# Kernel optimization log

Measured on AMD Instinct MI355X. Metric: run time of the kernel, lower is better.

The kernel has to match this reference:

```python
import jax, jax.numpy as jnp
import numpy as np

N = 50000       # nodes
E = 800000      # edges (avg degree 16)
F_IN = 128      # in_feats
H = 128         # h_feats
C = 16          # num_classes
EPS = 1e-5      # BatchNorm eps


def setup_inputs() -> dict:
    key = jax.random.key(0)
    ks = jax.random.split(key, 26)
    rn = lambda k, shape: jax.random.normal(k, shape, dtype=jnp.float32) * 0.05
    zeros = lambda d: jnp.zeros((d,), jnp.float32)
    ones = lambda d: jnp.ones((d,), jnp.float32)
    return {
        "features": jax.random.normal(ks[0], (N, F_IN), dtype=jnp.float32),
        "src": jax.random.randint(ks[1], (E,), 0, N),
        "dst": jax.random.randint(ks[2], (E,), 0, N),
        # input_encoder
        "W_in": rn(ks[3], (F_IN, H)), "b_in": zeros(H),
        # SAGEConv layer 0: H -> 2H (fc_self, fc_neigh, bias)
        "Ws0": rn(ks[4], (H, 2 * H)), "Wn0": rn(ks[5], (H, 2 * H)), "bs0": zeros(2 * H),
        # BatchNorm1d(2H) eval-mode stats
        "g0": ones(2 * H), "bt0": zeros(2 * H),
        "m0": rn(ks[6], (2 * H,)),
        "v0": jax.random.uniform(ks[7], (2 * H,), jnp.float32, 0.5, 1.5),
        # SAGEConv layer 1: 2H -> H
        "Ws1": rn(ks[8], (2 * H, H)), "Wn1": rn(ks[9], (2 * H, H)), "bs1": zeros(H),
        # BatchNorm1d(H)
        "g1": ones(H), "bt1": zeros(H),
        "m1": rn(ks[10], (H,)),
        "v1": jax.random.uniform(ks[11], (H,), jnp.float32, 0.5, 1.5),
        # relation_encoder: 2H -> H
        "Wr": rn(ks[12], (2 * H, H)), "br": zeros(H),
        # classifier: H -> H//2 -> C
        "Wc1": rn(ks[13], (H, H // 2)), "bc1": zeros(H // 2),
        "Wc2": rn(ks[14], (H // 2, C)), "bc2": zeros(C),
    }


def _bn(x, g, b, m, v):
    # eval-mode BatchNorm1d with running stats
    return (x - m) * jax.lax.rsqrt(v + EPS) * g + b


def _sage(h, src, dst, Ws, Wn, b, inv_deg):
    # DGL SAGEConv 'mean': out = fc_self(h_dst) + fc_neigh(mean_{u in N(v)} h_u) + bias
    neigh = jax.ops.segment_sum(h[src], dst, num_segments=N) * inv_deg  # [N, d_in]
    return h @ Ws + neigh @ Wn + b


def reference(features, src, dst, W_in, b_in, Ws0, Wn0, bs0, g0, bt0, m0, v0,
              Ws1, Wn1, bs1, g1, bt1, m1, v1, Wr, br, Wc1, bc1, Wc2, bc2):
    deg = jax.ops.segment_sum(jnp.ones((E,), jnp.float32), dst, num_segments=N)
    inv_deg = (1.0 / jnp.maximum(deg, 1.0))[:, None]  # [N, 1]

    h0 = jax.nn.relu(features @ W_in + b_in)                       # [N, H]
    h = jax.nn.relu(_bn(_sage(h0, src, dst, Ws0, Wn0, bs0, inv_deg), g0, bt0, m0, v0))  # [N, 2H]
    h = jax.nn.relu(_bn(_sage(h, src, dst, Ws1, Wn1, bs1, inv_deg), g1, bt1, m1, v1))   # [N, H]

    h_final = jax.nn.relu(jnp.concatenate([h0, h], axis=1) @ Wr + br)  # [N, H]
    return jax.nn.relu(h_final @ Wc1 + bc1) @ Wc2 + bc2                # [N, C]
```

## Files before the change

### kernel.cpp

```cpp
#include <hip/hip_runtime.h>

typedef short v8s __attribute__((ext_vector_type(8)));
typedef float v4f __attribute__((ext_vector_type(4)));
typedef unsigned short u16;
typedef unsigned int u32;

#define NNODES 50000
#define NEDGES 800000
#define CSTRIDE 64

#define NB 512
#define BSPAN 98
#define EBLK 98
#define NBU 511
#define SUBCAP 48

__device__ __forceinline__ float bf2f(u16 b) {
    u32 u = ((u32)b) << 16;
    return __builtin_bit_cast(float, u);
}
__device__ __forceinline__ u16 f2bf(float f) {
    u32 u = __builtin_bit_cast(u32, f);
    u32 r = (u + 0x7fffu + ((u >> 16) & 1u)) >> 16;
    return (u16)r;
}

struct PackDesc { const float* B1; const float* B2; int K1, K2, N, csplit, start; u16* out; };
struct PackArgs { PackDesc d[6]; int total; };

__global__ __launch_bounds__(256) void prep_pack(
    PackArgs pa,
    const float* b_in, const float* bs0, const float* g0, const float* bt0,
    const float* m0, const float* v0,
    const float* bs1, const float* g1, const float* bt1, const float* m1, const float* v1,
    const float* br, const float* bc1, const float* bc2,
    float* sc_in, float* sh_in, float* sc0, float* sh0, float* sc1, float* sh1,
    float* sc_r, float* sh_r, float* sh_c1, float* sh_c2) {
    int t = threadIdx.x;
    if (blockIdx.x == 0) {
        if (t < 128) { sc_in[t] = 1.f; sh_in[t] = b_in[t]; }
        if (t < 256) {
            float s = g0[t] * rsqrtf(v0[t] + 1e-5f);
            sc0[t] = s;
            sh0[t] = (bs0[t] - m0[t]) * s + bt0[t];
        }
        if (t < 128) {
            float s = g1[t] * rsqrtf(v1[t] + 1e-5f);
            sc1[t] = s;
            sh1[t] = (bs1[t] - m1[t]) * s + bt1[t];
        }
        if (t < 128) { sc_r[t] = 1.f; sh_r[t] = br[t]; }
        if (t < 64)  { sh_c1[t] = bc1[t]; }
        if (t < 16)  { sh_c2[t] = bc2[t]; }
    }
    int tid = blockIdx.x * 256 + t;
    if (tid >= pa.total) return;
    int s = 0;
    for (int i = 1; i < 6; i++)
        if (tid >= pa.d[i].start) s = i;
    const PackDesc& D = pa.d[s];
    int tt = tid - D.start;
    int frag = tt >> 9;
    int rem = tt & 511;
    int lane = rem >> 3;
    int j = rem & 7;
    int nf = D.N >> 4;
    int kt = frag / nf, nt = frag - kt * nf;
    int k = kt * 32 + (lane >> 4) * 8 + j;
    int n = nt * 16 + (lane & 15);
    float v;
    if (D.csplit)
        v = (n < D.csplit) ? D.B1[(size_t)k * D.csplit + n]
                           : D.B2[(size_t)k * (D.N - D.csplit) + (n - D.csplit)];
    else
        v = (k < D.K1) ? D.B1[(size_t)k * D.N + n]
                       : D.B2[(size_t)(k - D.K1) * D.N + n];
    D.out[tt] = f2bf(v);
}

template <int BN, int CW, int KT, int KSPLIT, bool RELU, bool F32OUT, bool AF32>
__device__ __forceinline__ void gemm_body(
    int bx,
    const void* __restrict__ A0v, int lda0,
    const void* __restrict__ A1v, int lda1,
    int M,
    const v8s* __restrict__ Bp,
    const float* __restrict__ scale, const float* __restrict__ shift,
    u16* __restrict__ C, float* __restrict__ Cf, int ldc) {
    constexpr int NFW = BN / 16 / CW;
    constexpr int RW = 4 / CW;
    int lane = threadIdx.x & 63;
    int wave = threadIdx.x >> 6;
    int colw = wave % CW;
    int roww = wave / CW;
    int quad = lane >> 4;
    int l16 = lane & 15;
    int base = bx * (64 * RW) + roww * 64;

    v4f acc[4][NFW];
#pragma unroll
    for (int rg = 0; rg < 4; rg++)
#pragma unroll
        for (int nt = 0; nt < NFW; nt++) acc[rg][nt] = (v4f)0.0f;

    size_t o0[4], o1[4];
#pragma unroll
    for (int rg = 0; rg < 4; rg++) {
        int r = base + rg * 16 + l16;
        if (r > M - 1) r = M - 1;
        o0[rg] = (size_t)r * lda0 + quad * 8;
        o1[rg] = (size_t)r * lda1 + quad * 8;
    }

    auto load_a = [&](const void* Av, size_t off) -> v8s {
        if constexpr (AF32) {
            const float* p = (const float*)Av + off;
            float4 x = *(const float4*)p;
            float4 y = *(const float4*)(p + 4);
            v8s a;
            a[0] = (short)f2bf(x.x); a[1] = (short)f2bf(x.y);
            a[2] = (short)f2bf(x.z); a[3] = (short)f2bf(x.w);
            a[4] = (short)f2bf(y.x); a[5] = (short)f2bf(y.y);
            a[6] = (short)f2bf(y.z); a[7] = (short)f2bf(y.w);
            return a;
        } else {
            return *(const v8s*)((const u16*)Av + off);
        }
    };

#pragma unroll
    for (int kt = 0; kt < KT; kt++) {
        v8s a[4];
#pragma unroll
        for (int rg = 0; rg < 4; rg++) {
            if (kt < KSPLIT) a[rg] = load_a(A0v, o0[rg] + kt * 32);
            else             a[rg] = load_a(A1v, o1[rg] + (size_t)(kt - KSPLIT) * 32);
        }
        const v8s* bb = Bp + (size_t)kt * (BN / 16) * 64 + (colw * NFW) * 64 + lane;
#pragma unroll
        for (int nt = 0; nt < NFW; nt++) {
            v8s b = bb[nt * 64];
#pragma unroll
            for (int rg = 0; rg < 4; rg++)
                acc[rg][nt] = __builtin_amdgcn_mfma_f32_16x16x32_bf16(a[rg], b, acc[rg][nt], 0, 0, 0);
        }
    }

    int colbase = colw * (NFW * 16);
#pragma unroll
    for (int rg = 0; rg < 4; rg++) {
        int rbase = base + rg * 16 + quad * 4;
#pragma unroll
        for (int nt = 0; nt < NFW; nt++) {
            int col = colbase + nt * 16 + l16;
            float s = scale[col], sh = shift[col];
#pragma unroll
            for (int i = 0; i < 4; i++) {
                int row = rbase + i;
                if (row < M) {
                    float v = acc[rg][nt][i] * s + sh;
                    if (RELU) v = v > 0.f ? v : 0.f;
                    if (F32OUT) Cf[(size_t)row * ldc + col] = v;
                    else C[(size_t)row * ldc + col] = f2bf(v);
                }
            }
        }
    }
}

__device__ __forceinline__ u32 gather_mean2(
    const u16* __restrict__ nl, int d, const u16* __restrict__ Hl, int ldh) {
    float a0 = 0.f, a1 = 0.f, b0 = 0.f, b1 = 0.f;
    float c0 = 0.f, c1 = 0.f, d0 = 0.f, d1 = 0.f;
    float e0 = 0.f, e1 = 0.f, f0 = 0.f, f1 = 0.f;
    float g0 = 0.f, g1 = 0.f, h0_ = 0.f, h1_ = 0.f;
    int e = 0;
    for (; e + 8 <= d; e += 8) {
        int u0 = nl[e], u1 = nl[e + 1], u2 = nl[e + 2], u3 = nl[e + 3];
        int u4 = nl[e + 4], u5 = nl[e + 5], u6 = nl[e + 6], u7 = nl[e + 7];
        u32 w0 = *(const u32*)(Hl + (size_t)u0 * ldh);
        u32 w1 = *(const u32*)(Hl + (size_t)u1 * ldh);
        u32 w2 = *(const u32*)(Hl + (size_t)u2 * ldh);
        u32 w3 = *(const u32*)(Hl + (size_t)u3 * ldh);
        u32 w4 = *(const u32*)(Hl + (size_t)u4 * ldh);
        u32 w5 = *(const u32*)(Hl + (size_t)u5 * ldh);
        u32 w6 = *(const u32*)(Hl + (size_t)u6 * ldh);
        u32 w7 = *(const u32*)(Hl + (size_t)u7 * ldh);
        a0 += bf2f((u16)w0); a1 += bf2f((u16)(w0 >> 16));
        b0 += bf2f((u16)w1); b1 += bf2f((u16)(w1 >> 16));
        c0 += bf2f((u16)w2); c1 += bf2f((u16)(w2 >> 16));
        d0 += bf2f((u16)w3); d1 += bf2f((u16)(w3 >> 16));
        e0 += bf2f((u16)w4); e1 += bf2f((u16)(w4 >> 16));
        f0 += bf2f((u16)w5); f1 += bf2f((u16)(w5 >> 16));
        g0 += bf2f((u16)w6); g1 += bf2f((u16)(w6 >> 16));
        h0_ += bf2f((u16)w7); h1_ += bf2f((u16)(w7 >> 16));
    }
    for (; e + 4 <= d; e += 4) {
        int u0 = nl[e], u1 = nl[e + 1], u2 = nl[e + 2], u3 = nl[e + 3];
        u32 w0 = *(const u32*)(Hl + (size_t)u0 * ldh);
        u32 w1 = *(const u32*)(Hl + (size_t)u1 * ldh);
        u32 w2 = *(const u32*)(Hl + (size_t)u2 * ldh);
        u32 w3 = *(const u32*)(Hl + (size_t)u3 * ldh);
        a0 += bf2f((u16)w0); a1 += bf2f((u16)(w0 >> 16));
        b0 += bf2f((u16)w1); b1 += bf2f((u16)(w1 >> 16));
        c0 += bf2f((u16)w2); c1 += bf2f((u16)(w2 >> 16));
        d0 += bf2f((u16)w3); d1 += bf2f((u16)(w3 >> 16));
    }
    for (; e < d; e++) {
        int u = nl[e];
        u32 w = *(const u32*)(Hl + (size_t)u * ldh);
        a0 += bf2f((u16)w); a1 += bf2f((u16)(w >> 16));
    }
    float s = 1.0f / (float)(d > 0 ? d : 1);
    float r0 = ((a0 + b0) + (c0 + d0)) + ((e0 + f0) + (g0 + h0_));
    float r1 = ((a1 + b1) + (c1 + d1)) + ((e1 + f1) + (g1 + h1_));
    return (u32)f2bf(r0 * s) | ((u32)f2bf(r1 * s) << 16);
}

__global__ __launch_bounds__(256) void mega_binA_h0(
    const int* __restrict__ src, const int* __restrict__ dst,
    int* __restrict__ gcnt, u32* __restrict__ gbuf,
    const float* __restrict__ features,
    const v8s* __restrict__ Winp,
    const float* __restrict__ sc_in, const float* __restrict__ sh_in,
    u16* __restrict__ hcat0) {
    int bx = blockIdx.x;
    if (bx < EBLK) {
        __shared__ int lcnt[NB];
        int t = threadIdx.x;
        for (int i = t; i < NB; i += 256) lcnt[i] = 0;
        __syncthreads();
        int ebase = bx * 8192;
#pragma unroll
        for (int c = 0; c < 8; c++) {
            int e0 = ebase + c * 1024 + t * 4;
            if (e0 + 4 <= NEDGES) {
                int4 s4 = *(const int4*)(src + e0);
                int4 d4 = *(const int4*)(dst + e0);
                int ss[4] = {s4.x, s4.y, s4.z, s4.w};
                int dd[4] = {d4.x, d4.y, d4.z, d4.w};
#pragma unroll
                for (int j = 0; j < 4; j++) {
                    int b = dd[j] / BSPAN;
                    int dl = dd[j] - b * BSPAN;
                    int p = atomicAdd(&lcnt[b], 1);
                    if (p < SUBCAP)
                        gbuf[((size_t)b * EBLK + bx) * SUBCAP + p] =
                            ((u32)dl << 16) | (u32)ss[j];
                }
            } else {
#pragma unroll
                for (int j = 0; j < 4; j++) {
                    int e = e0 + j;
                    if (e < NEDGES) {
                        int d = dst[e];
                        int b = d / BSPAN;
                        int dl = d - b * BSPAN;
                        int p = atomicAdd(&lcnt[b], 1);
                        if (p < SUBCAP)
                            gbuf[((size_t)b * EBLK + bx) * SUBCAP + p] =
                                ((u32)dl << 16) | (u32)src[e];
                    }
                }
            }
        }
        __syncthreads();
        for (int i = t; i < NB; i += 256) {
            int c = lcnt[i];
            if (c > SUBCAP) c = SUBCAP;
            gcnt[bx * NB + i] = c;
        }
    } else {
        gemm_body<128, 4, 4, 4, true, false, true>(
            bx - EBLK, features, 128, features, 128, NNODES,
            Winp, sc_in, sh_in, hcat0, nullptr, 256);
    }
}

__global__ __launch_bounds__(1024) void fill_bg(
    const u32* __restrict__ gbuf, const int* __restrict__ gcnt,
    u16* __restrict__ csr, int* __restrict__ cursor,
    const u16* __restrict__ H, u16* __restrict__ D) {
    __shared__ u16 lcsr[BSPAN * CSTRIDE];
    __shared__ int lcur[BSPAN];
    __shared__ int scnt[EBLK];
    int b = blockIdx.x;
    int t = threadIdx.x;
    int v0 = b * BSPAN;
    int span = NNODES - v0;
    if (span > BSPAN) span = BSPAN;
    for (int i = t; i < BSPAN; i += 1024) lcur[i] = 0;
    for (int i = t; i < EBLK; i += 1024) scnt[i] = gcnt[i * NB + b];
    __syncthreads();
    const u32* gb = gbuf + (size_t)b * EBLK * SUBCAP;
    for (int s = t; s < EBLK * SUBCAP; s += 1024) {
        int blk = s / SUBCAP;
        int idx = s - blk * SUBCAP;
        if (idx < scnt[blk]) {
            u32 pk = gb[s];
            int dl = pk >> 16;
            int p = atomicAdd(&lcur[dl], 1);
            if (p < CSTRIDE) lcsr[(dl << 6) + p] = (u16)(pk & 0xffffu);
        }
    }
    __syncthreads();
    {
        const u32* lw = (const u32*)lcsr;
        u32* gw = (u32*)(csr + ((size_t)v0 << 6));
        int nw = span * (CSTRIDE / 2);
        for (int i = t; i < nw; i += 1024) gw[i] = lw[i];
        for (int i = t; i < span; i += 1024) cursor[v0 + i] = lcur[i];
    }
    int lane = t & 63;
    int wv = t >> 6;
    for (int i = wv; i < span; i += 16) {
        int d = lcur[i];
        if (d > CSTRIDE) d = CSTRIDE;
        u32 o = gather_mean2(&lcsr[i << 6], d, H + lane * 2, 256);
        *(u32*)(D + (size_t)(v0 + i) * 256 + lane * 2) = o;
    }
}

__global__ __launch_bounds__(256) void gemm_h1ps(
    const u16* __restrict__ A,
    const v8s* __restrict__ B0,
    const float* __restrict__ sc0, const float* __restrict__ sh0,
    const v8s* __restrict__ B1,
    u16* __restrict__ ps, int M) {
    constexpr int LSTR = 264;
    __shared__ u16 h1s[64 * LSTR];
    int lane = threadIdx.x & 63;
    int wave = threadIdx.x >> 6;
    int quad = lane >> 4;
    int l16 = lane & 15;
    int base = blockIdx.x * 64;

    v4f acc[4][4];
#pragma unroll
    for (int rg = 0; rg < 4; rg++)
#pragma unroll
        for (int nt = 0; nt < 4; nt++) acc[rg][nt] = (v4f)0.0f;

    size_t o0[4];
#pragma unroll
    for (int rg = 0; rg < 4; rg++) {
        int r = base + rg * 16 + l16;
        if (r > M - 1) r = M - 1;
        o0[rg] = (size_t)r * 256 + quad * 8;
    }

#pragma unroll
    for (int kt = 0; kt < 8; kt++) {
        v8s a[4];
#pragma unroll
        for (int rg = 0; rg < 4; rg++) a[rg] = *(const v8s*)(A + o0[rg] + kt * 32);
        const v8s* bb = B0 + (size_t)kt * 16 * 64 + (wave * 4) * 64 + lane;
#pragma unroll
        for (int nt = 0; nt < 4; nt++) {
            v8s b = bb[nt * 64];
#pragma unroll
            for (int rg = 0; rg < 4; rg++)
                acc[rg][nt] = __builtin_amdgcn_mfma_f32_16x16x32_bf16(a[rg], b, acc[rg][nt], 0, 0, 0);
        }
    }
    int colbase = wave * 64;
#pragma unroll
    for (int rg = 0; rg < 4; rg++) {
        int rowL = rg * 16 + quad * 4;
#pragma unroll
        for (int nt = 0; nt < 4; nt++) {
            int col = colbase + nt * 16 + l16;
            float s = sc0[col], sh = sh0[col];
#pragma unroll
            for (int i = 0; i < 4; i++) {
                float v = acc[rg][nt][i] * s + sh;
                v = v > 0.f ? v : 0.f;
                h1s[(rowL + i) * LSTR + col] = f2bf(v);
            }
        }
    }
    __syncthreads();

#pragma unroll
    for (int rg = 0; rg < 4; rg++)
#pragma unroll
        for (int nt = 0; nt < 4; nt++) acc[rg][nt] = (v4f)0.0f;
#pragma unroll
    for (int kt = 0; kt < 8; kt++) {
        v8s a[4];
#pragma unroll
        for (int rg = 0; rg < 4; rg++)
            a[rg] = *(const v8s*)(&h1s[(rg * 16 + l16) * LSTR + quad * 8 + kt * 32]);
        const v8s* bb = B1 + (size_t)kt * 16 * 64 + (wave * 4) * 64 + lane;
#pragma unroll
        for (int nt = 0; nt < 4; nt++) {
            v8s b = bb[nt * 64];
#pragma unroll
            for (int rg = 0; rg < 4; rg++)
                acc[rg][nt] = __builtin_amdgcn_mfma_f32_16x16x32_bf16(a[rg], b, acc[rg][nt], 0, 0, 0);
        }
    }
#pragma unroll
    for (int rg = 0; rg < 4; rg++) {
        int rbase = base + rg * 16 + quad * 4;
#pragma unroll
        for (int nt = 0; nt < 4; nt++) {
            int col = colbase + nt * 16 + l16;
#pragma unroll
            for (int i = 0; i < 4; i++) {
                int row = rbase + i;
                if (row < M) ps[(size_t)row * 256 + col] = f2bf(acc[rg][nt][i]);
            }
        }
    }
}

__global__ __launch_bounds__(256) void agg_h2(
    const int* __restrict__ cursor, const u16* __restrict__ csr,
    const u16* __restrict__ ps,
    const float* __restrict__ sc1, const float* __restrict__ sh1,
    u16* __restrict__ h2, int n) {
    int v = blockIdx.x * 4 + (threadIdx.x >> 6);
    if (v >= n) return;
    int lane = threadIdx.x & 63;
    int d = cursor[v];
    if (d > CSTRIDE) d = CSTRIDE;
    u32 sv = *(const u32*)(ps + (size_t)v * 256 + lane * 2);
    u32 nm = gather_mean2(csr + ((size_t)v << 6), d, ps + 128 + lane * 2, 256);
    int col = lane * 2;
    float x0 = (bf2f((u16)sv) + bf2f((u16)nm)) * sc1[col] + sh1[col];
    float x1 = (bf2f((u16)(sv >> 16)) + bf2f((u16)(nm >> 16))) * sc1[col + 1] + sh1[col + 1];
    x0 = x0 > 0.f ? x0 : 0.f;
    x1 = x1 > 0.f ? x1 : 0.f;
    u32 o = (u32)f2bf(x0) | ((u32)f2bf(x1) << 16);
    *(u32*)(h2 + (size_t)v * 128 + lane * 2) = o;
}

__global__ __launch_bounds__(256) void gemm_chain(
    const u16* __restrict__ hcat0,
    const u16* __restrict__ h2,
    const v8s* __restrict__ Wrp, const float* __restrict__ sc_r, const float* __restrict__ sh_r,
    const v8s* __restrict__ Wm1p, const float* __restrict__ sh_c1,
    const v8s* __restrict__ Wm2p, const float* __restrict__ sh_c2,
    float* __restrict__ out, int M) {
    constexpr int LS = 136;
    __shared__ u16 tile[64 * LS];
    int lane = threadIdx.x & 63;
    int wv = threadIdx.x >> 6;
    int quad = lane >> 4;
    int l16 = lane & 15;
    int base = blockIdx.x * 64;

    v4f acc[4][2];
#pragma unroll
    for (int rg = 0; rg < 4; rg++)
#pragma unroll
        for (int nt = 0; nt < 2; nt++) acc[rg][nt] = (v4f)0.0f;
    size_t o0[4], o1[4];
#pragma unroll
    for (int rg = 0; rg < 4; rg++) {
        int r = base + rg * 16 + l16;
        if (r > M - 1) r = M - 1;
        o0[rg] = (size_t)r * 256 + quad * 8;
        o1[rg] = (size_t)r * 128 + quad * 8;
    }
#pragma unroll
    for (int kt = 0; kt < 8; kt++) {
        v8s a[4];
#pragma unroll
        for (int rg = 0; rg < 4; rg++) {
            if (kt < 4) a[rg] = *(const v8s*)(hcat0 + o0[rg] + kt * 32);
            else        a[rg] = *(const v8s*)(h2 + o1[rg] + (size_t)(kt - 4) * 32);
        }
        const v8s* bb = Wrp + (size_t)kt * 8 * 64 + (wv * 2) * 64 + lane;
#pragma unroll
        for (int nt = 0; nt < 2; nt++) {
            v8s b = bb[nt * 64];
#pragma unroll
            for (int rg = 0; rg < 4; rg++)
                acc[rg][nt] = __builtin_amdgcn_mfma_f32_16x16x32_bf16(a[rg], b, acc[rg][nt], 0, 0, 0);
        }
    }
    {
        int colbase = wv * 32;
#pragma unroll
        for (int rg = 0; rg < 4; rg++) {
            int rowL = rg * 16 + quad * 4;
#pragma unroll
            for (int nt = 0; nt < 2; nt++) {
                int col = colbase + nt * 16 + l16;
                float s = sc_r[col], sh = sh_r[col];
#pragma unroll
                for (int i = 0; i < 4; i++) {
                    float v = acc[rg][nt][i] * s + sh;
                    v = v > 0.f ? v : 0.f;
                    tile[(rowL + i) * LS + col] = f2bf(v);
                }
            }
        }
    }
    __syncthreads();

    v4f a2[4];
#pragma unroll
    for (int rg = 0; rg < 4; rg++) a2[rg] = (v4f)0.0f;
#pragma unroll
    for (int kt = 0; kt < 4; kt++) {
        v8s a[4];
#pragma unroll
        for (int rg = 0; rg < 4; rg++)
            a[rg] = *(const v8s*)(&tile[(rg * 16 + l16) * LS + quad * 8 + kt * 32]);
        v8s b = Wm1p[(size_t)kt * 4 * 64 + wv * 64 + lane];
#pragma unroll
        for (int rg = 0; rg < 4; rg++)
            a2[rg] = __builtin_amdgcn_mfma_f32_16x16x32_bf16(a[rg], b, a2[rg], 0, 0, 0);
    }
    __syncthreads();
    {
        int col = wv * 16 + l16;
        float sh = sh_c1[col];
#pragma unroll
        for (int rg = 0; rg < 4; rg++) {
            int rowL = rg * 16 + quad * 4;
#pragma unroll
            for (int i = 0; i < 4; i++) {
                float v = a2[rg][i] + sh;
                v = v > 0.f ? v : 0.f;
                tile[(rowL + i) * LS + col] = f2bf(v);
            }
        }
    }
    __syncthreads();

    v4f a3 = (v4f)0.0f;
#pragma unroll
    for (int kt = 0; kt < 2; kt++) {
        v8s a = *(const v8s*)(&tile[(wv * 16 + l16) * LS + quad * 8 + kt * 32]);
        v8s b = Wm2p[kt * 64 + lane];
        a3 = __builtin_amdgcn_mfma_f32_16x16x32_bf16(a, b, a3, 0, 0, 0);
    }
    int row = base + wv * 16 + quad * 4;
    float sh = sh_c2[l16];
#pragma unroll
    for (int i = 0; i < 4; i++) {
        int r = row + i;
        if (r < M) out[(size_t)r * 16 + l16] = a3[i] + sh;
    }
}

extern "C" void kernel_launch(void* const* d_in, const int* in_sizes, int n_in,
                              void* d_out, int out_size, void* d_ws, size_t ws_size,
                              hipStream_t stream) {
    const int N = NNODES;
    const float* features = (const float*)d_in[0];
    const int* src = (const int*)d_in[1];
    const int* dst = (const int*)d_in[2];
    float* out = (float*)d_out;

    char* w = (char*)d_ws;
    auto alloc = [&](size_t bytes) -> char* {
        char* p = w;
        w += (bytes + 255) & ~(size_t)255;
        return p;
    };
    int*   cursor = (int*)alloc((size_t)N * 4);
    u16*   csr    = (u16*)alloc((size_t)N * CSTRIDE * 2);
    u16*   hcat0  = (u16*)alloc((size_t)N * 256 * 2);
    u16*   ps     = (u16*)alloc((size_t)N * 256 * 2);
    u16*   h2     = (u16*)alloc((size_t)N * 128 * 2);
    u32*   gbuf   = (u32*)alloc((size_t)NBU * EBLK * SUBCAP * 4);
    int*   gcnt   = (int*)alloc((size_t)EBLK * NB * 4);
    u16*   Winp   = (u16*)alloc(128 * 128 * 2);
    u16*   Wc0p   = (u16*)alloc(256 * 256 * 2);
    u16*   Wsn1p  = (u16*)alloc(256 * 256 * 2);
    u16*   Wrp    = (u16*)alloc(256 * 128 * 2);
    u16*   Wm1p   = (u16*)alloc(128 * 64 * 2);
    u16*   Wm2p   = (u16*)alloc(64 * 16 * 2);
    float* sc_in = (float*)alloc(128 * 4); float* sh_in = (float*)alloc(128 * 4);
    float* sc0   = (float*)alloc(256 * 4); float* sh0   = (float*)alloc(256 * 4);
    float* sc1   = (float*)alloc(128 * 4); float* sh1   = (float*)alloc(128 * 4);
    float* sc_r  = (float*)alloc(128 * 4); float* sh_r  = (float*)alloc(128 * 4);
    float* sh_c1 = (float*)alloc(64 * 4);
    float* sh_c2 = (float*)alloc(16 * 4);

    PackArgs pa;
    int st = 0;
    auto seg = [&](int i, const float* B1, const float* B2, int K1, int K2,
                   int Nn, int csp, u16* o) {
        pa.d[i] = {B1, B2, K1, K2, Nn, csp, st, o};
        st += (K1 + K2) * Nn;
    };
    seg(0, (const float*)d_in[3], nullptr, 128, 0, 128, 0, Winp);
    seg(1, (const float*)d_in[5], (const float*)d_in[6], 128, 128, 256, 0, Wc0p);
    seg(2, (const float*)d_in[12], (const float*)d_in[13], 256, 0, 256, 128, Wsn1p);
    seg(3, (const float*)d_in[19], nullptr, 256, 0, 128, 0, Wrp);
    seg(4, (const float*)d_in[21], nullptr, 128, 0, 64, 0, Wm1p);
    seg(5, (const float*)d_in[23], nullptr, 64, 0, 16, 0, Wm2p);
    pa.total = st;

    prep_pack<<<(st + 255) / 256, 256, 0, stream>>>(
        pa,
        (const float*)d_in[4], (const float*)d_in[7], (const float*)d_in[8],
        (const float*)d_in[9], (const float*)d_in[10], (const float*)d_in[11],
        (const float*)d_in[14], (const float*)d_in[15], (const float*)d_in[16],
        (const float*)d_in[17], (const float*)d_in[18], (const float*)d_in[20],
        (const float*)d_in[22], (const float*)d_in[24],
        sc_in, sh_in, sc0, sh0, sc1, sh1, sc_r, sh_r, sh_c1, sh_c2);

    int gb64 = (N + 63) / 64;
    mega_binA_h0<<<EBLK + gb64, 256, 0, stream>>>(
        src, dst, gcnt, gbuf, features, (const v8s*)Winp, sc_in, sh_in, hcat0);
    fill_bg<<<NBU, 1024, 0, stream>>>(gbuf, gcnt, csr, cursor, hcat0, hcat0 + 128);
    gemm_h1ps<<<gb64, 256, 0, stream>>>(hcat0, (const v8s*)Wc0p, sc0, sh0,
                                        (const v8s*)Wsn1p, ps, N);
    agg_h2<<<(N + 3) / 4, 256, 0, stream>>>(cursor, csr, ps, sc1, sh1, h2, N);
    gemm_chain<<<gb64, 256, 0, stream>>>(
        hcat0, h2, (const v8s*)Wrp, sc_r, sh_r,
        (const v8s*)Wm1p, sh_c1, (const v8s*)Wm2p, sh_c2, out, N);
}
```

Measured before the change: 257.8 us.

## Fuse layer-0 neighbor mean into the bucket fill kernel with the two GEMMs

```diff
diff --git a/kernel.cpp b/kernel.cpp
--- a/kernel.cpp
+++ b/kernel.cpp
@@ -166,6 +166,33 @@
             }
         }
     }
+}
+
+__device__ __forceinline__ u32 gather_mean2_l(
+    const u16* __restrict__ nl, int d, const u16* __restrict__ Hl, int ldh) {
+    float a0 = 0.f, a1 = 0.f, b0 = 0.f, b1 = 0.f;
+    float c0 = 0.f, c1 = 0.f, d0 = 0.f, d1 = 0.f;
+    int e = 0;
+    for (; e + 4 <= d; e += 4) {
+        int u0 = nl[e], u1 = nl[e + 1], u2 = nl[e + 2], u3 = nl[e + 3];
+        u32 w0 = *(const u32*)(Hl + (size_t)u0 * ldh);
+        u32 w1 = *(const u32*)(Hl + (size_t)u1 * ldh);
+        u32 w2 = *(const u32*)(Hl + (size_t)u2 * ldh);
+        u32 w3 = *(const u32*)(Hl + (size_t)u3 * ldh);
+        a0 += bf2f((u16)w0); a1 += bf2f((u16)(w0 >> 16));
+        b0 += bf2f((u16)w1); b1 += bf2f((u16)(w1 >> 16));
+        c0 += bf2f((u16)w2); c1 += bf2f((u16)(w2 >> 16));
+        d0 += bf2f((u16)w3); d1 += bf2f((u16)(w3 >> 16));
+    }
+    for (; e < d; e++) {
+        int u = nl[e];
+        u32 w = *(const u32*)(Hl + (size_t)u * ldh);
+        a0 += bf2f((u16)w); a1 += bf2f((u16)(w >> 16));
+    }
+    float s = 1.0f / (float)(d > 0 ? d : 1);
+    float r0 = (a0 + b0) + (c0 + d0);
+    float r1 = (a1 + b1) + (c1 + d1);
+    return (u32)f2bf(r0 * s) | ((u32)f2bf(r1 * s) << 16);
 }
 
 __device__ __forceinline__ u32 gather_mean2(
@@ -223,7 +250,7 @@
     const float* __restrict__ features,
     const v8s* __restrict__ Winp,
     const float* __restrict__ sc_in, const float* __restrict__ sh_in,
-    u16* __restrict__ hcat0) {
+    u16* __restrict__ h0) {
     int bx = blockIdx.x;
     if (bx < EBLK) {
         __shared__ int lcnt[NB];
@@ -273,22 +300,31 @@
     } else {
         gemm_body<128, 4, 4, 4, true, false, true>(
             bx - EBLK, features, 128, features, 128, NNODES,
-            Winp, sc_in, sh_in, hcat0, nullptr, 256);
-    }
-}
-
-__global__ __launch_bounds__(1024) void fill_bg(
+            Winp, sc_in, sh_in, h0, nullptr, 128);
+    }
+}
+
+__global__ __launch_bounds__(1024, 8) void fill_bgg(
     const u32* __restrict__ gbuf, const int* __restrict__ gcnt,
     u16* __restrict__ csr, int* __restrict__ cursor,
-    const u16* __restrict__ H, u16* __restrict__ D) {
+    const u16* __restrict__ h0,
+    const v8s* __restrict__ B0,
+    const float* __restrict__ sc0, const float* __restrict__ sh0,
+    const v8s* __restrict__ B1,
+    u16* __restrict__ ps) {
+    constexpr int NLS = 136;
+    constexpr int LSTR = 264;
     __shared__ u16 lcsr[BSPAN * CSTRIDE];
     __shared__ int lcur[BSPAN];
     __shared__ int scnt[EBLK];
+    __shared__ u16 n0s[BSPAN * NLS];
+    __shared__ u16 h1s[64 * LSTR];
     int b = blockIdx.x;
     int t = threadIdx.x;
     int v0 = b * BSPAN;
     int span = NNODES - v0;
     if (span > BSPAN) span = BSPAN;
+
     for (int i = t; i < BSPAN; i += 1024) lcur[i] = 0;
     for (int i = t; i < EBLK; i += 1024) scnt[i] = gcnt[i * NB + b];
     __syncthreads();
@@ -311,107 +347,84 @@
         for (int i = t; i < nw; i += 1024) gw[i] = lw[i];
         for (int i = t; i < span; i += 1024) cursor[v0 + i] = lcur[i];
     }
+
     int lane = t & 63;
-    int wv = t >> 6;
-    for (int i = wv; i < span; i += 16) {
+    int colw = t >> 6;
+    for (int i = colw; i < span; i += 16) {
         int d = lcur[i];
         if (d > CSTRIDE) d = CSTRIDE;
-        u32 o = gather_mean2(&lcsr[i << 6], d, H + lane * 2, 256);
-        *(u32*)(D + (size_t)(v0 + i) * 256 + lane * 2) = o;
-    }
-}
-
-__global__ __launch_bounds__(256) void gemm_h1ps(
-    const u16* __restrict__ A,
-    const v8s* __restrict__ B0,
-    const float* __restrict__ sc0, const float* __restrict__ sh0,
-    const v8s* __restrict__ B1,
-    u16* __restrict__ ps, int M) {
-    constexpr int LSTR = 264;
-    __shared__ u16 h1s[64 * LSTR];
-    int lane = threadIdx.x & 63;
-    int wave = threadIdx.x >> 6;
+        u32 o = gather_mean2_l(&lcsr[i << 6], d, h0 + lane * 2, 128);
+        *(u32*)(&n0s[i * NLS + lane * 2]) = o;
+    }
+    __syncthreads();
+
     int quad = lane >> 4;
     int l16 = lane & 15;
-    int base = blockIdx.x * 64;
-
-    v4f acc[4][4];
-#pragma unroll
-    for (int rg = 0; rg < 4; rg++)
-#pragma unroll
-        for (int nt = 0; nt < 4; nt++) acc[rg][nt] = (v4f)0.0f;
-
-    size_t o0[4];
-#pragma unroll
-    for (int rg = 0; rg < 4; rg++) {
-        int r = base + rg * 16 + l16;
-        if (r > M - 1) r = M - 1;
-        o0[rg] = (size_t)r * 256 + quad * 8;
-    }
-
-#pragma unroll
-    for (int kt = 0; kt < 8; kt++) {
-        v8s a[4];
-#pragma unroll
-        for (int rg = 0; rg < 4; rg++) a[rg] = *(const v8s*)(A + o0[rg] + kt * 32);
-        const v8s* bb = B0 + (size_t)kt * 16 * 64 + (wave * 4) * 64 + lane;
-#pragma unroll
-        for (int nt = 0; nt < 4; nt++) {
-            v8s b = bb[nt * 64];
-#pragma unroll
-            for (int rg = 0; rg < 4; rg++)
-                acc[rg][nt] = __builtin_amdgcn_mfma_f32_16x16x32_bf16(a[rg], b, acc[rg][nt], 0, 0, 0);
-        }
-    }
-    int colbase = wave * 64;
-#pragma unroll
-    for (int rg = 0; rg < 4; rg++) {
-        int rowL = rg * 16 + quad * 4;
-#pragma unroll
-        for (int nt = 0; nt < 4; nt++) {
-            int col = colbase + nt * 16 + l16;
-            float s = sc0[col], sh = sh0[col];
-#pragma unroll
-            for (int i = 0; i < 4; i++) {
-                float v = acc[rg][nt][i] * s + sh;
-                v = v > 0.f ? v : 0.f;
-                h1s[(rowL + i) * LSTR + col] = f2bf(v);
-            }
-        }
-    }
-    __syncthreads();
-
-#pragma unroll
-    for (int rg = 0; rg < 4; rg++)
-#pragma unroll
-        for (int nt = 0; nt < 4; nt++) acc[rg][nt] = (v4f)0.0f;
-#pragma unroll
-    for (int kt = 0; kt < 8; kt++) {
-        v8s a[4];
-#pragma unroll
-        for (int rg = 0; rg < 4; rg++)
-            a[rg] = *(const v8s*)(&h1s[(rg * 16 + l16) * LSTR + quad * 8 + kt * 32]);
-        const v8s* bb = B1 + (size_t)kt * 16 * 64 + (wave * 4) * 64 + lane;
-#pragma unroll
-        for (int nt = 0; nt < 4; nt++) {
-            v8s b = bb[nt * 64];
-#pragma unroll
-            for (int rg = 0; rg < 4; rg++)
-                acc[rg][nt] = __builtin_amdgcn_mfma_f32_16x16x32_bf16(a[rg], b, acc[rg][nt], 0, 0, 0);
-        }
-    }
-#pragma unroll
-    for (int rg = 0; rg < 4; rg++) {
-        int rbase = base + rg * 16 + quad * 4;
-#pragma unroll
-        for (int nt = 0; nt < 4; nt++) {
-            int col = colbase + nt * 16 + l16;
-#pragma unroll
-            for (int i = 0; i < 4; i++) {
-                int row = rbase + i;
-                if (row < M) ps[(size_t)row * 256 + col] = f2bf(acc[rg][nt][i]);
-            }
-        }
+#pragma unroll
+    for (int s = 0; s < 2; s++) {
+        int rbase = s * 64;
+        int rlc[4];
+        size_t go[4];
+#pragma unroll
+        for (int rg = 0; rg < 4; rg++) {
+            int rl = rbase + rg * 16 + l16;
+            if (rl > span - 1) rl = span - 1;
+            rlc[rg] = rl;
+            go[rg] = (size_t)(v0 + rl) * 128 + quad * 8;
+        }
+        v4f acc[4];
+#pragma unroll
+        for (int rg = 0; rg < 4; rg++) acc[rg] = (v4f)0.0f;
+#pragma unroll
+        for (int kt = 0; kt < 8; kt++) {
+            v8s bfr = B0[(size_t)kt * 16 * 64 + colw * 64 + lane];
+#pragma unroll
+            for (int rg = 0; rg < 4; rg++) {
+                v8s a;
+                if (kt < 4) a = *(const v8s*)(h0 + go[rg] + kt * 32);
+                else        a = *(const v8s*)(&n0s[rlc[rg] * NLS + quad * 8 + (kt - 4) * 32]);
+                acc[rg] = __builtin_amdgcn_mfma_f32_16x16x32_bf16(a, bfr, acc[rg], 0, 0, 0);
+            }
+        }
+        {
+            int col = colw * 16 + l16;
+            float sc = sc0[col], sh = sh0[col];
+#pragma unroll
+            for (int rg = 0; rg < 4; rg++) {
+                int rowL = rg * 16 + quad * 4;
+#pragma unroll
+                for (int i = 0; i < 4; i++) {
+                    float v = acc[rg][i] * sc + sh;
+                    v = v > 0.f ? v : 0.f;
+                    h1s[(rowL + i) * LSTR + col] = f2bf(v);
+                }
+            }
+        }
+        __syncthreads();
+#pragma unroll
+        for (int rg = 0; rg < 4; rg++) acc[rg] = (v4f)0.0f;
+#pragma unroll
+        for (int kt = 0; kt < 8; kt++) {
+            v8s bfr = B1[(size_t)kt * 16 * 64 + colw * 64 + lane];
+#pragma unroll
+            for (int rg = 0; rg < 4; rg++) {
+                v8s a = *(const v8s*)(&h1s[(rg * 16 + l16) * LSTR + quad * 8 + kt * 32]);
+                acc[rg] = __builtin_amdgcn_mfma_f32_16x16x32_bf16(a, bfr, acc[rg], 0, 0, 0);
+            }
+        }
+        {
+            int col = colw * 16 + l16;
+#pragma unroll
+            for (int rg = 0; rg < 4; rg++) {
+                int lr = rbase + rg * 16 + quad * 4;
+#pragma unroll
+                for (int i = 0; i < 4; i++) {
+                    if (lr + i < span)
+                        ps[(size_t)(v0 + lr + i) * 256 + col] = f2bf(acc[rg][i]);
+                }
+            }
+        }
+        __syncthreads();
     }
 }
 
@@ -437,7 +450,7 @@
 }
 
 __global__ __launch_bounds__(256) void gemm_chain(
-    const u16* __restrict__ hcat0,
+    const u16* __restrict__ h0,
     const u16* __restrict__ h2,
     const v8s* __restrict__ Wrp, const float* __restrict__ sc_r, const float* __restrict__ sh_r,
     const v8s* __restrict__ Wm1p, const float* __restrict__ sh_c1,
@@ -456,21 +469,20 @@
     for (int rg = 0; rg < 4; rg++)
 #pragma unroll
         for (int nt = 0; nt < 2; nt++) acc[rg][nt] = (v4f)0.0f;
-    size_t o0[4], o1[4];
+    size_t o0[4];
 #pragma unroll
     for (int rg = 0; rg < 4; rg++) {
         int r = base + rg * 16 + l16;
         if (r > M - 1) r = M - 1;
-        o0[rg] = (size_t)r * 256 + quad * 8;
-        o1[rg] = (size_t)r * 128 + quad * 8;
+        o0[rg] = (size_t)r * 128 + quad * 8;
     }
 #pragma unroll
     for (int kt = 0; kt < 8; kt++) {
         v8s a[4];
 #pragma unroll
         for (int rg = 0; rg < 4; rg++) {
-            if (kt < 4) a[rg] = *(const v8s*)(hcat0 + o0[rg] + kt * 32);
-            else        a[rg] = *(const v8s*)(h2 + o1[rg] + (size_t)(kt - 4) * 32);
+            if (kt < 4) a[rg] = *(const v8s*)(h0 + o0[rg] + kt * 32);
+            else        a[rg] = *(const v8s*)(h2 + o0[rg] + (size_t)(kt - 4) * 32);
         }
         const v8s* bb = Wrp + (size_t)kt * 8 * 64 + (wv * 2) * 64 + lane;
 #pragma unroll
@@ -565,7 +577,7 @@
     };
     int*   cursor = (int*)alloc((size_t)N * 4);
     u16*   csr    = (u16*)alloc((size_t)N * CSTRIDE * 2);
-    u16*   hcat0  = (u16*)alloc((size_t)N * 256 * 2);
+    u16*   h0     = (u16*)alloc((size_t)N * 128 * 2);
     u16*   ps     = (u16*)alloc((size_t)N * 256 * 2);
     u16*   h2     = (u16*)alloc((size_t)N * 128 * 2);
     u32*   gbuf   = (u32*)alloc((size_t)NBU * EBLK * SUBCAP * 4);
@@ -609,12 +621,12 @@
 
     int gb64 = (N + 63) / 64;
     mega_binA_h0<<<EBLK + gb64, 256, 0, stream>>>(
-        src, dst, gcnt, gbuf, features, (const v8s*)Winp, sc_in, sh_in, hcat0);
-    fill_bg<<<NBU, 1024, 0, stream>>>(gbuf, gcnt, csr, cursor, hcat0, hcat0 + 128);
-    gemm_h1ps<<<gb64, 256, 0, stream>>>(hcat0, (const v8s*)Wc0p, sc0, sh0,
-                                        (const v8s*)Wsn1p, ps, N);
+        src, dst, gcnt, gbuf, features, (const v8s*)Winp, sc_in, sh_in, h0);
+    fill_bgg<<<NBU, 1024, 0, stream>>>(gbuf, gcnt, csr, cursor, h0,
+                                       (const v8s*)Wc0p, sc0, sh0,
+                                       (const v8s*)Wsn1p, ps);
     agg_h2<<<(N + 3) / 4, 256, 0, stream>>>(cursor, csr, ps, sc1, sh1, h2, N);
     gemm_chain<<<gb64, 256, 0, stream>>>(
-        hcat0, h2, (const v8s*)Wrp, sc_r, sh_r,
+        h0, h2, (const v8s*)Wrp, sc_r, sh_r,
         (const v8s*)Wm1p, sh_c1, (const v8s*)Wm2p, sh_c2, out, N);
 }
```

After: 271.3 us. +5.2%, slower.
